# Performance work log

Hardware: AMD Instinct MI355X
Metric: run time of the kernel (lower is better)

## Reference

```python
import jax, jax.numpy as jnp
import numpy as np

GRID_SIZE = 5
SPLINE_ORDER = 3
N_COEF = GRID_SIZE + SPLINE_ORDER  # 8
NUM_NODES = 100000
NUM_EDGES = 1200000
NUM_GRAPHS = 512
D = 64
N_TARGETS = 10


def _grid():
    # uniform grid on [-1, 1] extended by spline_order knots on each side (efficient-kan default)
    h = 2.0 / GRID_SIZE
    return jnp.arange(-SPLINE_ORDER, GRID_SIZE + SPLINE_ORDER + 1, dtype=jnp.float32) * h - 1.0


def b_splines(x):
    # x: (N, in) -> (N, in, N_COEF) via Cox-de Boor recursion
    g = _grid()
    xe = x[..., None]
    bases = ((xe >= g[:-1]) & (xe < g[1:])).astype(x.dtype)
    for k in range(1, SPLINE_ORDER + 1):
        left = (xe - g[: -(k + 1)]) / (g[k:-1] - g[: -(k + 1)])
        right = (g[k + 1:] - xe) / (g[k + 1:] - g[1:-k])
        bases = left * bases[..., :-1] + right * bases[..., 1:]
    return bases


def kan_linear(x, base_w, spline_w, scaler):
    # efficient-kan KANLinear: silu base branch + standalone-scaled spline branch
    base = jax.nn.silu(x) @ base_w.T
    sb = b_splines(x)  # (N, in, N_COEF)
    spline = jnp.einsum('nig,oig->no', sb, spline_w * scaler[..., None])
    return base + spline


def setup_inputs() -> dict:
    key = jax.random.key(0)
    ks = jax.random.split(key, 12)
    inp = {
        'x': jax.random.normal(ks[0], (NUM_NODES, D), dtype=jnp.float32),
        'edge_index': jax.random.randint(ks[1], (2, NUM_EDGES), 0, NUM_NODES, dtype=jnp.int64),
        'batch': jnp.sort(jax.random.randint(ks[2], (NUM_NODES,), 0, NUM_GRAPHS, dtype=jnp.int64)),
        # GINConv layer 0 KAN (D -> D)
        'base_w0': jax.random.normal(ks[3], (D, D), dtype=jnp.float32) * 0.1,
        'spline_w0': jax.random.normal(ks[4], (D, D, N_COEF), dtype=jnp.float32) * 0.1,
        'scaler0': jax.random.normal(ks[5], (D, D), dtype=jnp.float32) * 0.1 + 1.0,
        # GINConv layer 1 KAN (D -> D)
        'base_w1': jax.random.normal(ks[6], (D, D), dtype=jnp.float32) * 0.1,
        'spline_w1': jax.random.normal(ks[7], (D, D, N_COEF), dtype=jnp.float32) * 0.1,
        'scaler1': jax.random.normal(ks[8], (D, D), dtype=jnp.float32) * 0.1 + 1.0,
        # head KAN (D -> N_TARGETS)
        'base_wh': jax.random.normal(ks[9], (N_TARGETS, D), dtype=jnp.float32) * 0.1,
        'spline_wh': jax.random.normal(ks[10], (N_TARGETS, D, N_COEF), dtype=jnp.float32) * 0.1,
        'scaler_h': jax.random.normal(ks[11], (N_TARGETS, D), dtype=jnp.float32) * 0.1 + 1.0,
    }
    return inp


def reference(x, edge_index, batch, base_w0, spline_w0, scaler0,
              base_w1, spline_w1, scaler1, base_wh, spline_wh, scaler_h):
    src, dst = edge_index[0], edge_index[1]
    n = x.shape[0]
    # GINConv layer 0: nn((1+eps)*x + sum_{j in N(i)} x_j), eps=0; dropout is eval-mode identity
    agg = jax.ops.segment_sum(x[src], dst, num_segments=n)
    h = kan_linear(x + agg, base_w0, spline_w0, scaler0)
    # GINConv layer 1
    agg = jax.ops.segment_sum(h[src], dst, num_segments=n)
    h = kan_linear(h + agg, base_w1, spline_w1, scaler1)
    # global_add_pool over graphs, then KAN head
    pooled = jax.ops.segment_sum(h, batch, num_segments=NUM_GRAPHS)
    return kan_linear(pooled, base_wh, spline_wh, scaler_h)
```

## Files before the change

kernel.cpp:

```cpp
#include <hip/hip_runtime.h>
#include <hip/hip_fp16.h>
#include <math.h>

#define NODES   100000
#define EDGES   1200000
#define GRAPHS  512
#define DIM     64
#define NT      10
#define KTOT    576

#define NB      512
#define NBUSED  391
#define EPB     4096
#define CAP     4608

#define KSTAGE     96
#define WTL_STRIDE 104
#define V_STRIDE   72

#define PREP_BLOCKS 288

typedef _Float16 f16x8  __attribute__((ext_vector_type(8)));
typedef __fp16   fp16x2 __attribute__((ext_vector_type(2)));
typedef __attribute__((ext_vector_type(4))) float frag_cd;

__device__ __forceinline__ float silu(float x) {
    return x / (1.f + __expf(-x));
}

__device__ __forceinline__ unsigned packh2(float a, float b) {
    fp16x2 h = __builtin_amdgcn_cvt_pkrtz(a, b);
    return __builtin_bit_cast(unsigned, h);
}

__device__ __forceinline__ void acc_h8(float* a, uint4 p) {
    union { uint4 u; __half2 h[4]; } up; up.u = p;
#pragma unroll
    for (int j = 0; j < 4; ++j) {
        float2 f = __half22float2(up.h[j]);
        a[2 * j]     += f.x;
        a[2 * j + 1] += f.y;
    }
}

__device__ __forceinline__ f16x8 bases_frag(float xv) {
    float tt  = fmaf(xv, 2.5f, 5.5f);
    float fm  = floorf(tt);
    int   m   = (int)fm;
    float u   = tt - fm;
    float um1 = 1.f - u;
    float v3  = u * u * u * (1.f / 6.f);
    float v0  = um1 * um1 * um1 * (1.f / 6.f);
    float B2m1 = 0.5f * ((u + 1.f) * um1 + (2.f - u) * u);
    float v1  = ((u + 2.f) * um1 * um1 * 0.5f + (2.f - u) * B2m1) * (1.f / 3.f);
    float v2  = ((u + 1.f) * B2m1 + (3.f - u) * u * u * 0.5f) * (1.f / 3.f);

    unsigned d0 = packh2(v0, v1);
    unsigned d1 = packh2(v2, v3);
    int p = m - 3;
    int B = p >> 1;
    bool odd = (p & 1) != 0;
    unsigned e1 = __builtin_amdgcn_alignbit(d1, d0, 16);
    unsigned W0 = odd ? (d0 << 16) : d0;
    unsigned W1 = odd ? e1 : d1;
    unsigned W2 = odd ? (d1 >> 16) : 0u;
    union { f16x8 f; unsigned u[4]; } r;
    r.u[0] = (B == 0) ? W0 : ((B == -1) ? W1 : ((B == -2) ? W2 : 0u));
    r.u[1] = (B == 1) ? W0 : ((B ==  0) ? W1 : ((B == -1) ? W2 : 0u));
    r.u[2] = (B == 2) ? W0 : ((B ==  1) ? W1 : ((B ==  0) ? W2 : 0u));
    r.u[3] = (B == 3) ? W0 : ((B ==  2) ? W1 : ((B ==  1) ? W2 : 0u));
    return r.f;
}

__global__ void prep_conv(const float* __restrict__ bw0, const float* __restrict__ sw0,
                          const float* __restrict__ sc0,
                          const float* __restrict__ bw1, const float* __restrict__ sw1,
                          const float* __restrict__ sc1,
                          unsigned short* __restrict__ wt0,
                          unsigned short* __restrict__ wt1,
                          const float* __restrict__ x, const int* __restrict__ bat,
                          unsigned short* __restrict__ xb,
                          unsigned short* __restrict__ hpad,
                          int* __restrict__ goff) {
    int bx = blockIdx.x;
    if (bx < PREP_BLOCKS) {
        int idx = bx * 256 + threadIdx.x;
        int layer = idx >= DIM * KTOT;
        int li = layer ? idx - DIM * KTOT : idx;
        const float* bw = layer ? bw1 : bw0;
        const float* sw = layer ? sw1 : sw0;
        const float* sc = layer ? sc1 : sc0;
        unsigned short* wt = layer ? wt1 : wt0;
        int o = li / KTOT, k = li % KTOT;
        float v;
        if (k < DIM) {
            v = bw[o * DIM + k];
        } else {
            int i = (k - DIM) >> 3, g = (k - DIM) & 7;
            v = sw[(o * DIM + i) * 8 + g] * sc[o * DIM + i];
        }
        wt[li] = __half_as_ushort(__float2half(v));
        return;
    }
    int i = (bx - PREP_BLOCKS) * 256 + threadIdx.x;
    if (i < NODES * 16) {
        float4 v = ((const float4*)x)[i];
        unsigned lo = packh2(v.x, v.y);
        unsigned hi = packh2(v.z, v.w);
        ((uint2*)xb)[i] = make_uint2(lo, hi);
        if ((i & 15) == 0) {
            int n = i >> 4;
            int b  = bat[n];
            int bp = (n == 0) ? -1 : bat[n - 1];
            for (int g = bp + 1; g <= b; ++g) goff[g] = n;
        }
        if (i == 0) {
            int blast = bat[NODES - 1];
            for (int g = blast + 1; g <= GRAPHS; ++g) goff[g] = NODES;
        }
    } else {
        int j = i - NODES * 16;
        if (j < 16)      ((uint2*)xb)[NODES * 16 + j] = make_uint2(0, 0);
        else if (j < 32) ((uint2*)hpad)[j - 16]       = make_uint2(0, 0);
    }
}

__global__ __launch_bounds__(256) void s3_partition(const int* __restrict__ ei,
                                                    int* __restrict__ bcur,
                                                    unsigned* __restrict__ tmp) {
    __shared__ int hist[NB], gbase[NB], cur[NB];
    int t = threadIdx.x;
    hist[t] = 0; hist[t + 256] = 0;
    cur[t]  = 0; cur[t + 256]  = 0;
    __syncthreads();
    int e0 = blockIdx.x * EPB;
#pragma unroll
    for (int k = 0; k < 16; ++k) {
        int e = e0 + t + k * 256;
        if (e < EDGES) atomicAdd(&hist[ei[EDGES + e] >> 8], 1);
    }
    __syncthreads();
    {
        int c0 = hist[t];       if (c0) gbase[t]       = atomicAdd(&bcur[t], c0);
        int c1 = hist[t + 256]; if (c1) gbase[t + 256] = atomicAdd(&bcur[t + 256], c1);
    }
    __syncthreads();
#pragma unroll
    for (int k = 0; k < 16; ++k) {
        int e = e0 + t + k * 256;
        if (e < EDGES) {
            unsigned src = (unsigned)ei[e];
            int dst = ei[EDGES + e];
            int b = dst >> 8;
            int slot = atomicAdd(&cur[b], 1);
            tmp[(size_t)b * CAP + gbase[b] + slot] = src | ((unsigned)(dst & 255) << 24);
        }
    }
}

__global__ __launch_bounds__(256) void s4_fill(const unsigned* __restrict__ tmp,
                                               const int* __restrict__ bcur,
                                               int2* __restrict__ rowp,
                                               int* __restrict__ col) {
    __shared__ int hist[256], scan[256], startsh[256];
    int b = blockIdx.x, t = threadIdx.x;
    int cnt = bcur[b];
    int base = b * CAP;
    hist[t] = 0;
    __syncthreads();
    for (int i = t; i < cnt; i += 256)
        atomicAdd(&hist[tmp[base + i] >> 24], 1);
    __syncthreads();
    int deg = hist[t];
    int pad = (deg + 3) & ~3;
    scan[t] = pad;
    __syncthreads();
    int run = pad;
    for (int d = 1; d < 256; d <<= 1) {
        int a = (t >= d) ? scan[t - d] : 0;
        __syncthreads();
        run += a; scan[t] = run;
        __syncthreads();
    }
    int start = base + run - pad;
    int ng = b * 256 + t;
    if (ng < NODES) rowp[ng] = make_int2(start, start + pad);
    __syncthreads();
    scan[t]    = start;
    startsh[t] = start;
    __syncthreads();
    for (int i = t; i < cnt; i += 256) {
        unsigned p = tmp[base + i];
        int pos = atomicAdd(&scan[p >> 24], 1);
        col[pos] = (int)(p & 0xFFFFFFu);
    }
    __syncthreads();
    for (int k = scan[t]; k < startsh[t] + pad; ++k) col[k] = NODES;
}

__global__ __launch_bounds__(256) void fused_layer(const unsigned short* __restrict__ xin,
                                                   const int2* __restrict__ rowp,
                                                   const int* __restrict__ col,
                                                   const unsigned short* __restrict__ wt,
                                                   unsigned short* __restrict__ out) {
    __shared__ unsigned short wt_lds[64 * WTL_STRIDE];
    __shared__ unsigned short v_lds[64 * V_STRIDE];

    const int t     = threadIdx.x;
    const int nbase = blockIdx.x * 64;

    uint4 p0, p1, p2;
    {
        int c0 = t, c1 = t + 256, c2 = t + 512;
        p0 = *(const uint4*)(wt + (c0 / 12) * KTOT + (c0 % 12) * 8);
        p1 = *(const uint4*)(wt + (c1 / 12) * KTOT + (c1 % 12) * 8);
        p2 = *(const uint4*)(wt + (c2 / 12) * KTOT + (c2 % 12) * 8);
    }

    const uint4* x4 = (const uint4*)xin;
#pragma unroll
    for (int rd = 0; rd < 2; ++rd) {
        int idx  = t + rd * 256;
        int node = idx >> 3, c8 = idx & 7;
        int n = nbase + node;
        uint4 res = make_uint4(0, 0, 0, 0);
        if (n < NODES) {
            int2 be = rowp[n];
            float a0[8], a1[8], a2[8], a3[8];
#pragma unroll
            for (int j = 0; j < 8; ++j) { a0[j] = 0.f; a1[j] = 0.f; a2[j] = 0.f; a3[j] = 0.f; }
            acc_h8(a0, x4[(size_t)n * 8 + c8]);
            for (int p = be.x; p < be.y; p += 4) {
                int c0 = col[p];
                int c1 = col[p + 1];
                int c2 = col[p + 2];
                int c3 = col[p + 3];
                uint4 r0 = x4[(size_t)c0 * 8 + c8];
                uint4 r1 = x4[(size_t)c1 * 8 + c8];
                uint4 r2 = x4[(size_t)c2 * 8 + c8];
                uint4 r3 = x4[(size_t)c3 * 8 + c8];
                acc_h8(a0, r0); acc_h8(a1, r1); acc_h8(a2, r2); acc_h8(a3, r3);
            }
            union { uint4 u; unsigned w[4]; } rr;
#pragma unroll
            for (int j = 0; j < 4; ++j) {
                float lo = a0[2 * j]     + a1[2 * j]     + a2[2 * j]     + a3[2 * j];
                float hi = a0[2 * j + 1] + a1[2 * j + 1] + a2[2 * j + 1] + a3[2 * j + 1];
                rr.w[j] = packh2(lo, hi);
            }
            res = rr.u;
        }
        *(uint4*)(v_lds + node * V_STRIDE + c8 * 8) = res;
    }
    {
        int c0 = t, c1 = t + 256, c2 = t + 512;
        *(uint4*)(wt_lds + (c0 / 12) * WTL_STRIDE + (c0 % 12) * 8) = p0;
        *(uint4*)(wt_lds + (c1 / 12) * WTL_STRIDE + (c1 % 12) * 8) = p1;
        *(uint4*)(wt_lds + (c2 / 12) * WTL_STRIDE + (c2 % 12) * 8) = p2;
    }
    __syncthreads();

    const int w = t >> 6;
    const int l = t & 63;
    const int q = l >> 4;
    const int c = l & 15;
    const unsigned short* vrow = v_lds + ((w << 4) + c) * V_STRIDE;

    frag_cd ac0 = {0.f, 0.f, 0.f, 0.f};
    frag_cd ac1 = {0.f, 0.f, 0.f, 0.f};
    frag_cd ac2 = {0.f, 0.f, 0.f, 0.f};
    frag_cd ac3 = {0.f, 0.f, 0.f, 0.f};

#define MSTEP(OFF, A) {                                                          \
        f16x8 b0 = *(const f16x8*)(wt_lds + (c     ) * WTL_STRIDE + (OFF));      \
        f16x8 b1 = *(const f16x8*)(wt_lds + (c + 16) * WTL_STRIDE + (OFF));      \
        f16x8 b2 = *(const f16x8*)(wt_lds + (c + 32) * WTL_STRIDE + (OFF));      \
        f16x8 b3 = *(const f16x8*)(wt_lds + (c + 48) * WTL_STRIDE + (OFF));      \
        ac0 = __builtin_amdgcn_mfma_f32_16x16x32_f16(A, b0, ac0, 0, 0, 0);       \
        ac1 = __builtin_amdgcn_mfma_f32_16x16x32_f16(A, b1, ac1, 0, 0, 0);       \
        ac2 = __builtin_amdgcn_mfma_f32_16x16x32_f16(A, b2, ac2, 0, 0, 0);       \
        ac3 = __builtin_amdgcn_mfma_f32_16x16x32_f16(A, b3, ac3, 0, 0, 0); }

    {
        int c0 = t, c1 = t + 256, c2 = t + 512;
        p0 = *(const uint4*)(wt + (c0 / 12) * KTOT + KSTAGE + (c0 % 12) * 8);
        p1 = *(const uint4*)(wt + (c1 / 12) * KTOT + KSTAGE + (c1 % 12) * 8);
        p2 = *(const uint4*)(wt + (c2 / 12) * KTOT + KSTAGE + (c2 % 12) * 8);
    }

#pragma unroll
    for (int s = 0; s < 2; ++s) {
        f16x8 hv = *(const f16x8*)(vrow + 32 * s + 8 * q);
        float f[8];
#pragma unroll
        for (int j = 0; j < 8; ++j) f[j] = silu((float)hv[j]);
        union { f16x8 v; unsigned u[4]; } a;
#pragma unroll
        for (int j = 0; j < 4; ++j) a.u[j] = packh2(f[2 * j], f[2 * j + 1]);
        MSTEP(32 * s + 8 * q, a.v);
    }
    {
        f16x8 a = bases_frag((float)(*(const _Float16*)(vrow + q)));
        MSTEP(64 + 8 * q, a);
    }

#pragma unroll
    for (int st = 1; st < 6; ++st) {
        __syncthreads();
        {
            int c0 = t, c1 = t + 256, c2 = t + 512;
            *(uint4*)(wt_lds + (c0 / 12) * WTL_STRIDE + (c0 % 12) * 8) = p0;
            *(uint4*)(wt_lds + (c1 / 12) * WTL_STRIDE + (c1 % 12) * 8) = p1;
            *(uint4*)(wt_lds + (c2 / 12) * WTL_STRIDE + (c2 % 12) * 8) = p2;
        }
        __syncthreads();
        if (st < 5) {
            int c0 = t, c1 = t + 256, c2 = t + 512;
            p0 = *(const uint4*)(wt + (c0 / 12) * KTOT + (st + 1) * KSTAGE + (c0 % 12) * 8);
            p1 = *(const uint4*)(wt + (c1 / 12) * KTOT + (st + 1) * KSTAGE + (c1 % 12) * 8);
            p2 = *(const uint4*)(wt + (c2 / 12) * KTOT + (st + 1) * KSTAGE + (c2 % 12) * 8);
        }
#pragma unroll
        for (int k = 0; k < 3; ++k) {
            int s = 3 * st + k;
            f16x8 a = bases_frag((float)(*(const _Float16*)(vrow + 4 * s + q - 8)));
            MSTEP(32 * k + 8 * q, a);
        }
    }
#undef MSTEP

    const int n0 = nbase + (w << 4) + (q << 2);
#pragma unroll
    for (int r = 0; r < 4; ++r) {
        int n = n0 + r;
        if (n < NODES) {
            unsigned short* o = out + (size_t)n * DIM + c;
            o[0]  = __half_as_ushort(__float2half(ac0[r]));
            o[16] = __half_as_ushort(__float2half(ac1[r]));
            o[32] = __half_as_ushort(__float2half(ac2[r]));
            o[48] = __half_as_ushort(__float2half(ac3[r]));
        }
    }
}

__global__ __launch_bounds__(256) void pool_head(const unsigned short* __restrict__ h,
                                                 const int* __restrict__ goff,
                                                 const float* __restrict__ bwh,
                                                 const float* __restrict__ swh,
                                                 const float* __restrict__ sch,
                                                 float* __restrict__ out) {
    __shared__ float ps[8][64];
    const int g = blockIdx.x, t = threadIdx.x;
    const int start = goff[g], end = goff[g + 1];
    const int d2 = t & 31, grp = t >> 5;
    float s0 = 0.f, s1 = 0.f;
    for (int n = start + grp; n < end; n += 8) {
        __half2 hv = *(const __half2*)(h + (size_t)n * DIM + 2 * d2);
        float2 f = __half22float2(hv);
        s0 += f.x;
        s1 += f.y;
    }
    ps[grp][2 * d2]     = s0;
    ps[grp][2 * d2 + 1] = s1;
    __syncthreads();

    if (t < 64) {
        const int i = t;
        float xv = 0.f;
#pragma unroll
        for (int k = 0; k < 8; ++k) xv += ps[k][i];

        float s  = silu(xv);
        float tt  = fmaf(xv, 2.5f, 5.5f);
        float fm  = floorf(tt);
        int   m   = (int)fm;
        float u   = tt - fm;
        float um1 = 1.f - u;
        float v3  = u * u * u * (1.f / 6.f);
        float v0  = um1 * um1 * um1 * (1.f / 6.f);
        float B2m1 = 0.5f * ((u + 1.f) * um1 + (2.f - u) * u);
        float v1  = ((u + 2.f) * um1 * um1 * 0.5f + (2.f - u) * B2m1) * (1.f / 3.f);
        float v2  = ((u + 1.f) * B2m1 + (3.f - u) * u * u * 0.5f) * (1.f / 3.f);
        bool inr  = (m >= 0) && (m <= 10);
        float b[8];
#pragma unroll
        for (int j = 0; j < 8; ++j) {
            float bv = 0.f;
            bv = (j == m - 3) ? v0 : bv;
            bv = (j == m - 2) ? v1 : bv;
            bv = (j == m - 1) ? v2 : bv;
            bv = (j == m)     ? v3 : bv;
            b[j] = inr ? bv : 0.f;
        }

        float part[NT];
#pragma unroll
        for (int o = 0; o < NT; ++o) {
            const float* sp = swh + (o * DIM + i) * 8;
            float sb = 0.f;
#pragma unroll
            for (int qq = 0; qq < 8; ++qq) sb = fmaf(b[qq], sp[qq], sb);
            part[o] = fmaf(s, bwh[o * DIM + i], sb * sch[o * DIM + i]);
        }
#pragma unroll
        for (int o = 0; o < NT; ++o) {
            float v = part[o];
#pragma unroll
            for (int off = 32; off > 0; off >>= 1) v += __shfl_down(v, off, 64);
            if (i == 0) out[g * NT + o] = v;
        }
    }
}

extern "C" void kernel_launch(void* const* d_in, const int* in_sizes, int n_in,
                              void* d_out, int out_size, void* d_ws, size_t ws_size,
                              hipStream_t stream) {
    const float* x   = (const float*)d_in[0];
    const int*   ei  = (const int*)d_in[1];
    const int*   bat = (const int*)d_in[2];
    const float* bw0 = (const float*)d_in[3];
    const float* sw0 = (const float*)d_in[4];
    const float* sc0 = (const float*)d_in[5];
    const float* bw1 = (const float*)d_in[6];
    const float* sw1 = (const float*)d_in[7];
    const float* sc1 = (const float*)d_in[8];
    const float* bwh = (const float*)d_in[9];
    const float* swh = (const float*)d_in[10];
    const float* sch = (const float*)d_in[11];
    float* out = (float*)d_out;

    const size_t ROW = (size_t)(NODES + 1) * DIM;

    unsigned short* wt0 = (unsigned short*)d_ws;
    unsigned short* wt1 = wt0 + DIM * KTOT;
    unsigned short* xbf = wt1 + DIM * KTOT;
    unsigned short* hbf = xbf + ROW;
    unsigned short* h2  = hbf + ROW;
    int* goff     = (int*)(h2 + (size_t)NODES * DIM);
    int2* rowp    = (int2*)(goff + 514);
    int* col      = (int*)(rowp + NODES);
    int* bcur     = col + (size_t)NB * CAP;
    unsigned* tmp = (unsigned*)(bcur + NB);

    const int conv_blocks = (NODES * 16 + 32 + 255) / 256;
    prep_conv<<<PREP_BLOCKS + conv_blocks, 256, 0, stream>>>(
        bw0, sw0, sc0, bw1, sw1, sc1, wt0, wt1,
        x, bat, xbf, hbf + (size_t)NODES * DIM, goff);

    (void)hipMemsetAsync(bcur, 0, NB * sizeof(int), stream);
    const int part_blocks = (EDGES + EPB - 1) / EPB;
    s3_partition<<<part_blocks, 256, 0, stream>>>(ei, bcur, tmp);
    s4_fill<<<NBUSED, 256, 0, stream>>>(tmp, bcur, rowp, col);

    const int layer_blocks = (NODES + 63) / 64;
    fused_layer<<<layer_blocks, 256, 0, stream>>>(xbf, rowp, col, wt0, hbf);
    fused_layer<<<layer_blocks, 256, 0, stream>>>(hbf, rowp, col, wt1, h2);

    pool_head<<<GRAPHS, 256, 0, stream>>>(h2, goff, bwh, swh, sch, out);
}
```

Baseline: 232.6 us.

## Stage CSR columns in LDS for gather and coalesce CSR build writes

The partition kernel now keeps each edge's src/dst in registers instead of reading the edge list from global memory twice. The fill kernel builds each bucket's column list in LDS and writes it out with coalesced int4 stores, replacing scattered global stores. The fused layer kernel preloads the block's contiguous column span into LDS when it fits and reads neighbor indices as int4, cutting per-node global index loads. The costs are more LDS, which may lower occupancy, an extra barrier, and a duplicated fallback path for large spans.

```diff
diff --git a/kernel.cpp b/kernel.cpp
--- a/kernel.cpp
+++ b/kernel.cpp
@@ -13,6 +13,7 @@
 #define NBUSED  391
 #define EPB     4096
 #define CAP     4608
+#define COLBUF  2048
 
 #define KSTAGE     96
 #define WTL_STRIDE 104
@@ -134,10 +135,14 @@
     cur[t]  = 0; cur[t + 256]  = 0;
     __syncthreads();
     int e0 = blockIdx.x * EPB;
+    int src[16], dst[16];
 #pragma unroll
     for (int k = 0; k < 16; ++k) {
         int e = e0 + t + k * 256;
-        if (e < EDGES) atomicAdd(&hist[ei[EDGES + e] >> 8], 1);
+        bool valid = e < EDGES;
+        src[k] = valid ? ei[e] : 0;
+        dst[k] = valid ? ei[EDGES + e] : -1;
+        if (valid) atomicAdd(&hist[dst[k] >> 8], 1);
     }
     __syncthreads();
     {
@@ -147,13 +152,11 @@
     __syncthreads();
 #pragma unroll
     for (int k = 0; k < 16; ++k) {
-        int e = e0 + t + k * 256;
-        if (e < EDGES) {
-            unsigned src = (unsigned)ei[e];
-            int dst = ei[EDGES + e];
-            int b = dst >> 8;
+        if (dst[k] >= 0) {
+            int b = dst[k] >> 8;
             int slot = atomicAdd(&cur[b], 1);
-            tmp[(size_t)b * CAP + gbase[b] + slot] = src | ((unsigned)(dst & 255) << 24);
+            tmp[(size_t)b * CAP + gbase[b] + slot] =
+                (unsigned)src[k] | ((unsigned)(dst[k] & 255) << 24);
         }
     }
 }
@@ -162,7 +165,9 @@
                                                const int* __restrict__ bcur,
                                                int2* __restrict__ rowp,
                                                int* __restrict__ col) {
-    __shared__ int hist[256], scan[256], startsh[256];
+    __shared__ int hist[256], scan[256], tot;
+    __shared__ int4 colbuf4[CAP / 4];
+    int* colbuf = (int*)colbuf4;
     int b = blockIdx.x, t = threadIdx.x;
     int cnt = bcur[b];
     int base = b * CAP;
@@ -182,20 +187,24 @@
         run += a; scan[t] = run;
         __syncthreads();
     }
-    int start = base + run - pad;
+    int start = run - pad;
     int ng = b * 256 + t;
-    if (ng < NODES) rowp[ng] = make_int2(start, start + pad);
-    __syncthreads();
-    scan[t]    = start;
-    startsh[t] = start;
+    if (ng < NODES) rowp[ng] = make_int2(base + start, base + start + pad);
+    if (t == 255) tot = run;
+    __syncthreads();
+    scan[t] = start;
     __syncthreads();
     for (int i = t; i < cnt; i += 256) {
         unsigned p = tmp[base + i];
         int pos = atomicAdd(&scan[p >> 24], 1);
-        col[pos] = (int)(p & 0xFFFFFFu);
-    }
-    __syncthreads();
-    for (int k = scan[t]; k < startsh[t] + pad; ++k) col[k] = NODES;
+        colbuf[pos] = (int)(p & 0xFFFFFFu);
+    }
+    __syncthreads();
+    for (int k = scan[t]; k < start + pad; ++k) colbuf[k] = NODES;
+    __syncthreads();
+    int nq = tot >> 2;
+    int4* out4 = (int4*)(col + base);
+    for (int i = t; i < nq; i += 256) out4[i] = colbuf4[i];
 }
 
 __global__ __launch_bounds__(256) void fused_layer(const unsigned short* __restrict__ xin,
@@ -205,6 +214,8 @@
                                                    unsigned short* __restrict__ out) {
     __shared__ unsigned short wt_lds[64 * WTL_STRIDE];
     __shared__ unsigned short v_lds[64 * V_STRIDE];
+    __shared__ int4 col4_lds[COLBUF / 4];
+    __shared__ int cinfo[2];
 
     const int t     = threadIdx.x;
     const int nbase = blockIdx.x * 64;
@@ -216,6 +227,23 @@
         p1 = *(const uint4*)(wt + (c1 / 12) * KTOT + (c1 % 12) * 8);
         p2 = *(const uint4*)(wt + (c2 / 12) * KTOT + (c2 % 12) * 8);
     }
+
+    if (t == 0) {
+        int cbeg = rowp[nbase].x;
+        int last = nbase + 63 < NODES ? nbase + 63 : NODES - 1;
+        int cend = rowp[last].y;
+        cinfo[0] = cbeg;
+        cinfo[1] = cend - cbeg;
+    }
+    __syncthreads();
+    const int cbeg = cinfo[0];
+    const int span = cinfo[1];
+    const bool lds_cols = (span <= COLBUF);
+    if (lds_cols) {
+        const int4* g4 = (const int4*)(col + cbeg);
+        for (int i = t; i < (span >> 2); i += 256) col4_lds[i] = g4[i];
+    }
+    __syncthreads();
 
     const uint4* x4 = (const uint4*)xin;
 #pragma unroll
@@ -229,17 +257,25 @@
             float a0[8], a1[8], a2[8], a3[8];
 #pragma unroll
             for (int j = 0; j < 8; ++j) { a0[j] = 0.f; a1[j] = 0.f; a2[j] = 0.f; a3[j] = 0.f; }
-            acc_h8(a0, x4[(size_t)n * 8 + c8]);
-            for (int p = be.x; p < be.y; p += 4) {
-                int c0 = col[p];
-                int c1 = col[p + 1];
-                int c2 = col[p + 2];
-                int c3 = col[p + 3];
-                uint4 r0 = x4[(size_t)c0 * 8 + c8];
-                uint4 r1 = x4[(size_t)c1 * 8 + c8];
-                uint4 r2 = x4[(size_t)c2 * 8 + c8];
-                uint4 r3 = x4[(size_t)c3 * 8 + c8];
-                acc_h8(a0, r0); acc_h8(a1, r1); acc_h8(a2, r2); acc_h8(a3, r3);
+            acc_h8(a0, x4[n * 8 + c8]);
+            if (lds_cols) {
+                for (int p = be.x; p < be.y; p += 4) {
+                    int4 c4 = *(const int4*)((const int*)col4_lds + (p - cbeg));
+                    uint4 r0 = x4[c4.x * 8 + c8];
+                    uint4 r1 = x4[c4.y * 8 + c8];
+                    uint4 r2 = x4[c4.z * 8 + c8];
+                    uint4 r3 = x4[c4.w * 8 + c8];
+                    acc_h8(a0, r0); acc_h8(a1, r1); acc_h8(a2, r2); acc_h8(a3, r3);
+                }
+            } else {
+                for (int p = be.x; p < be.y; p += 4) {
+                    int4 c4 = *(const int4*)(col + p);
+                    uint4 r0 = x4[c4.x * 8 + c8];
+                    uint4 r1 = x4[c4.y * 8 + c8];
+                    uint4 r2 = x4[c4.z * 8 + c8];
+                    uint4 r3 = x4[c4.w * 8 + c8];
+                    acc_h8(a0, r0); acc_h8(a1, r1); acc_h8(a2, r2); acc_h8(a3, r3);
+                }
             }
             union { uint4 u; unsigned w[4]; } rr;
 #pragma unroll
```

Result: faster. 224.7 us (-3.4%).
